# Performance work log

Measured on AMD Instinct MI355X. Metric: run time of the kernel, lower is better.

The kernel has to match this reference:

```python
import jax, jax.numpy as jnp
import numpy as np

NUM_EMBEDDINGS = 1_000_000
EMBEDDING_DIM = 64


def setup_inputs() -> dict:
    key = jax.random.key(0)
    k_idx, k_tab = jax.random.split(key)
    indices = jax.random.randint(k_idx, (16384, 50), 0, NUM_EMBEDDINGS, dtype=jnp.int64)
    # Shards are initialized with randn * (1/sqrt(dim)) and are row-contiguous
    # (shard s covers rows [s*shard_size, ...)), so a single concatenated table
    # is numerically identical.
    table = jax.random.normal(k_tab, (NUM_EMBEDDINGS, EMBEDDING_DIM), dtype=jnp.float32)
    table = table * (1.0 / jnp.sqrt(jnp.float32(EMBEDDING_DIM)))
    return {"indices": indices, "table": table}


def reference(indices, table):
    # forward: flatten, lookup rows (dedup/shard routing is an implementation
    # detail that is mathematically a pure gather), reshape to [..., dim].
    flat = indices.reshape(-1)
    emb = jnp.take(table, flat, axis=0)  # [N, dim]
    return emb.reshape(indices.shape + (table.shape[1],))
```

## Files before the change

### kernel.cpp

```cpp
#include <hip/hip_runtime.h>


__global__ __launch_bounds__(256) void ShardedCXLEmbedding_gather(
    const int* __restrict__ indices,
    const float4* __restrict__ table,
    float4* __restrict__ out,
    int n_rows)
{
    int g = blockIdx.x * 256 + threadIdx.x;
    int row = g >> 4;
    int c   = g & 15;
    if (row < n_rows) {
        int e = indices[row];
        out[g] = table[(long long)e * 16 + c];
    }
}

extern "C" void kernel_launch(void* const* d_in, const int* in_sizes, int n_in,
                              void* d_out, int out_size, void* d_ws, size_t ws_size,
                              hipStream_t stream) {
    const int*    indices = (const int*)d_in[0];
    const float4* table   = (const float4*)d_in[1];
    float4*       out     = (float4*)d_out;

    const int n_rows = in_sizes[0];
    const long long n_f4 = (long long)n_rows * 16;
    const int block = 256;
    const int grid  = (int)((n_f4 + block - 1) / block);

    ShardedCXLEmbedding_gather<<<grid, block, 0, stream>>>(indices, table, out, n_rows);
}
```

Baseline: 393.8 us.

## Use grid-stride gather with batched loads and nontemporal stores

Replaces the one-thread-per-float4 launch with a fixed 2048-block grid-stride loop. Each thread issues eight independent index and table loads before storing, which raises memory-level parallelism. Output is written with nontemporal stores so it does not pollute the cache. The risks are higher register use and fewer resident blocks, which may not fully saturate bandwidth.

```diff
diff --git a/kernel.cpp b/kernel.cpp
--- a/kernel.cpp
+++ b/kernel.cpp
@@ -1,32 +1,63 @@
 #include <hip/hip_runtime.h>
 
 
+typedef float vfloat4 __attribute__((ext_vector_type(4)));
+
+#define GATHER_BATCH 8
+
 __global__ __launch_bounds__(256) void ShardedCXLEmbedding_gather(
     const int* __restrict__ indices,
-    const float4* __restrict__ table,
-    float4* __restrict__ out,
-    int n_rows)
+    const vfloat4* __restrict__ table,
+    vfloat4* __restrict__ out,
+    int n_f4)
 {
+    const int stride = gridDim.x * 256;
     int g = blockIdx.x * 256 + threadIdx.x;
-    int row = g >> 4;
-    int c   = g & 15;
-    if (row < n_rows) {
-        int e = indices[row];
-        out[g] = table[(long long)e * 16 + c];
+
+    while (g + (GATHER_BATCH - 1) * stride < n_f4) {
+        int gs[GATHER_BATCH];
+        int es[GATHER_BATCH];
+        vfloat4 vs[GATHER_BATCH];
+
+        #pragma unroll
+        for (int k = 0; k < GATHER_BATCH; ++k) {
+            gs[k] = g + k * stride;
+            es[k] = indices[gs[k] >> 4];
+        }
+        #pragma unroll
+        for (int k = 0; k < GATHER_BATCH; ++k) {
+            vs[k] = table[(long long)es[k] * 16 + (gs[k] & 15)];
+        }
+        #pragma unroll
+        for (int k = 0; k < GATHER_BATCH; ++k) {
+            __builtin_nontemporal_store(vs[k], &out[gs[k]]);
+        }
+        g += GATHER_BATCH * stride;
+    }
+
+    while (g < n_f4) {
+        int e = indices[g >> 4];
+        vfloat4 v = table[(long long)e * 16 + (g & 15)];
+        __builtin_nontemporal_store(v, &out[g]);
+        g += stride;
     }
 }
 
 extern "C" void kernel_launch(void* const* d_in, const int* in_sizes, int n_in,
                               void* d_out, int out_size, void* d_ws, size_t ws_size,
                               hipStream_t stream) {
-    const int*    indices = (const int*)d_in[0];
-    const float4* table   = (const float4*)d_in[1];
-    float4*       out     = (float4*)d_out;
+    const int*     indices = (const int*)d_in[0];
+    const vfloat4* table   = (const vfloat4*)d_in[1];
+    vfloat4*       out     = (vfloat4*)d_out;
 
     const int n_rows = in_sizes[0];
     const long long n_f4 = (long long)n_rows * 16;
-    const int block = 256;
-    const int grid  = (int)((n_f4 + block - 1) / block);
 
-    ShardedCXLEmbedding_gather<<<grid, block, 0, stream>>>(indices, table, out, n_rows);
+    const int block  = 256;
+    int grid = 2048;
+    const long long work_blocks = (n_f4 + block - 1) / block;
+    if (work_blocks < grid) grid = (int)work_blocks;
+
+    ShardedCXLEmbedding_gather<<<grid, block, 0, stream>>>(
+        indices, table, out, (int)n_f4);
 }
```

Result: no change. 398.0 us (+1.1%).
